# Performance work log

Measured on AMD Instinct MI355X. Metric: run time of the kernel, lower is better.

## Reference

```python
import jax, jax.numpy as jnp
import numpy as np

B, S, D, L = 4, 512, 768, 64


def setup_inputs() -> dict:
    key = jax.random.key(0)
    k1, k2, k3, k4, k5 = jax.random.split(key, 5)
    return {
        "head": jax.random.normal(k1, (B, S, D), dtype=jnp.float32),
        "dep": jax.random.normal(k2, (B, S, D), dtype=jnp.float32),
        "label_U_diag": jax.random.normal(k3, (L, D), dtype=jnp.float32) * 0.02,
        "label_W": jax.random.normal(k4, (L, 2 * D), dtype=jnp.float32) * 0.02,
        "label_b": jax.random.normal(k5, (L,), dtype=jnp.float32) * 0.02,
    }


def reference(head, dep, label_U_diag, label_W, label_b):
    # t1[b,l,i,o] = sum_d head[b,i,d] * U[l,d] * dep[b,o,d]  (diag bilinear)
    t1 = jnp.einsum('bid,ld,bod->blio', head, label_U_diag, dep)
    # Linear term: instead of materializing the O(S^2 * 2D) concat tensor,
    # split W into head/dep halves and broadcast-add two O(S*L) matmuls.
    d = head.shape[-1]
    Wh, Wd = label_W[:, :d], label_W[:, d:]
    t2_h = jnp.einsum('bid,ld->bli', head, Wh)  # [B, L, S] (row / head index)
    t2_d = jnp.einsum('bod,ld->blo', dep, Wd)   # [B, L, S] (col / dep index)
    return t1 + t2_h[:, :, :, None] + t2_d[:, :, None, :] + label_b[None, :, None, None]
```

## Files before the change

kernel.cpp:

```cpp
#include <hip/hip_runtime.h>

typedef __bf16 bf16;
typedef __bf16 bf16x8 __attribute__((ext_vector_type(8)));
typedef float  f32x4  __attribute__((ext_vector_type(4)));

#define S 512
#define DD 768
#define LL 64
#define BB 4

__device__ __forceinline__ void async_copy16(const void* g, void* l) {
    __builtin_amdgcn_global_load_lds(
        (const __attribute__((address_space(1))) unsigned int*)g,
        (__attribute__((address_space(3))) unsigned int*)l,
        16, 0, 0);
}

__device__ __forceinline__ bf16x8 scale_cvt(float4 a, float4 b, float4 ua, float4 ub) {
    bf16x8 p;
    p[0] = (bf16)(a.x * ua.x); p[1] = (bf16)(a.y * ua.y);
    p[2] = (bf16)(a.z * ua.z); p[3] = (bf16)(a.w * ua.w);
    p[4] = (bf16)(b.x * ub.x); p[5] = (bf16)(b.y * ub.y);
    p[6] = (bf16)(b.z * ub.z); p[7] = (bf16)(b.w * ub.w);
    return p;
}

__global__ void cvt_dep_kernel(const float* __restrict__ dep, bf16* __restrict__ out) {
    int idx = (blockIdx.x * 256 + threadIdx.x) * 8;
    float4 a = *(const float4*)(dep + idx);
    float4 c = *(const float4*)(dep + idx + 4);
    bf16x8 p;
    p[0] = (bf16)a.x; p[1] = (bf16)a.y; p[2] = (bf16)a.z; p[3] = (bf16)a.w;
    p[4] = (bf16)c.x; p[5] = (bf16)c.y; p[6] = (bf16)c.z; p[7] = (bf16)c.w;
    *(bf16x8*)(out + idx) = p;
}

__global__ void t2_kernel(const float* __restrict__ head, const float* __restrict__ dep,
                          const float* __restrict__ W, const float* __restrict__ bias,
                          float* __restrict__ t2h, float* __restrict__ t2d) {
    __shared__ float Wl[16][DD];
    __shared__ float red[64][4][16];
    int bid = blockIdx.x;
    int sel = bid >> 7;
    int r   = bid & 127;
    int b   = r >> 5;
    int lg  = (r >> 3) & 3;
    int ic  = r & 7;
    const float* src = sel ? dep : head;
    int t = threadIdx.x;

    for (int l16 = 0; l16 < 16; ++l16) {
        const float* wp = W + (size_t)(lg * 16 + l16) * (2 * DD) + sel * DD;
        Wl[l16][t]       = wp[t];
        Wl[l16][t + 256] = wp[t + 256];
        Wl[l16][t + 512] = wp[t + 512];
    }
    __syncthreads();

    int iq = t >> 2, dq = t & 3;
    int i  = ic * 64 + iq;
    const float* rowp = src + (size_t)(b * S + i) * DD;
    float acc[16];
#pragma unroll
    for (int l16 = 0; l16 < 16; ++l16) acc[l16] = 0.f;
    for (int it = 0; it < 48; ++it) {
        int d = dq * 4 + it * 16;
        float4 x = *(const float4*)(rowp + d);
#pragma unroll
        for (int l16 = 0; l16 < 16; ++l16) {
            float4 wv = *(const float4*)&Wl[l16][d];
            acc[l16] += x.x * wv.x + x.y * wv.y + x.z * wv.z + x.w * wv.w;
        }
    }
#pragma unroll
    for (int l16 = 0; l16 < 16; ++l16) red[iq][dq][l16] = acc[l16];
    __syncthreads();

    int iq2 = t >> 2, l4 = t & 3;
    float* dst = sel ? t2d : t2h;
#pragma unroll
    for (int j = 0; j < 4; ++j) {
        int l16 = l4 * 4 + j;
        float v = red[iq2][0][l16] + red[iq2][1][l16] + red[iq2][2][l16] + red[iq2][3][l16];
        if (sel) v += bias[lg * 16 + l16];
        dst[(size_t)(b * LL + lg * 16 + l16) * S + ic * 64 + iq2] = v;
    }
}

__global__ __launch_bounds__(256, 2) void biaffine_main(
    const float* __restrict__ head, const bf16* __restrict__ depb,
    const float* __restrict__ U, const float* __restrict__ t2h,
    const float* __restrict__ t2d, float* __restrict__ out) {
    __shared__ __align__(16) bf16 As[128][32];
    __shared__ __align__(16) bf16 Bs[128][32];
    __shared__ __align__(16) float Ulds[DD];

    const int tid  = threadIdx.x;
    const int lane = tid & 63;
    const int w    = tid >> 6;
    const int bi0  = (blockIdx.x & 3) << 7;
    const int bo0  = (blockIdx.x >> 2) << 7;
    const int l    = blockIdx.y;
    const int b    = blockIdx.z;

    {
        const float* up = U + (size_t)l * DD;
        Ulds[tid]       = up[tid];
        Ulds[tid + 256] = up[tid + 256];
        Ulds[tid + 512] = up[tid + 512];
    }

    const int r1 = tid >> 2;
    const int cp = tid & 3;
    const int sw = (r1 >> 1) & 3;
    const int ca = cp ^ sw;
    const float* hp0 = head + (size_t)(b * S + bi0 + r1) * DD + ca * 8;
    const float* hp1 = hp0 + (size_t)64 * DD;
    bf16* awr0 = &As[r1][cp * 8];
    bf16* awr1 = &As[r1 + 64][cp * 8];

    const int rB0 = w * 32 + (lane >> 2);
    const int rB1 = rB0 + 16;
    const int cpB = lane & 3;
    const bf16* bp0 = depb + (size_t)(b * S + bo0 + rB0) * DD + (cpB ^ ((rB0 >> 1) & 3)) * 8;
    const bf16* bp1 = depb + (size_t)(b * S + bo0 + rB1) * DD + (cpB ^ ((rB1 >> 1) & 3)) * 8;
    bf16* bw0 = &Bs[w * 32][0];
    bf16* bw1 = &Bs[w * 32 + 16][0];

    const int wr = w & 1, wc = w >> 1;
    const int mrow = lane & 15, q = lane >> 4;
    const bf16* ap[4];
    const bf16* bp[4];
#pragma unroll
    for (int mi = 0; mi < 4; ++mi) {
        int rowA = wr * 64 + mi * 16 + mrow;
        ap[mi] = &As[rowA][(q ^ ((rowA >> 1) & 3)) * 8];
        int rowB = wc * 64 + mi * 16 + mrow;
        bp[mi] = &Bs[rowB][(q ^ ((rowB >> 1) & 3)) * 8];
    }

    f32x4 acc[4][4];
#pragma unroll
    for (int mi = 0; mi < 4; ++mi)
#pragma unroll
        for (int ni = 0; ni < 4; ++ni)
            acc[mi][ni] = (f32x4){0.f, 0.f, 0.f, 0.f};

    __syncthreads();

    const float* h0 = hp0;
    const float* h1 = hp1;
    const bf16*  g0 = bp0;
    const bf16*  g1 = bp1;
    for (int kt = 0; kt < 24; ++kt) {
        float4 h0a = *(const float4*)(h0);
        float4 h0b = *(const float4*)(h0 + 4);
        float4 h1a = *(const float4*)(h1);
        float4 h1b = *(const float4*)(h1 + 4);
        async_copy16(g0, bw0);
        async_copy16(g1, bw1);
        const float* uu = &Ulds[kt * 32 + ca * 8];
        float4 ua = *(const float4*)(uu);
        float4 ub = *(const float4*)(uu + 4);
        *(bf16x8*)awr0 = scale_cvt(h0a, h0b, ua, ub);
        *(bf16x8*)awr1 = scale_cvt(h1a, h1b, ua, ub);
        h0 += 32; h1 += 32; g0 += 32; g1 += 32;
        __syncthreads();

        bf16x8 af[4], bfr[4];
#pragma unroll
        for (int mi = 0; mi < 4; ++mi) af[mi]  = *(const bf16x8*)ap[mi];
#pragma unroll
        for (int ni = 0; ni < 4; ++ni) bfr[ni] = *(const bf16x8*)bp[ni];
#pragma unroll
        for (int mi = 0; mi < 4; ++mi)
#pragma unroll
            for (int ni = 0; ni < 4; ++ni)
                acc[mi][ni] = __builtin_amdgcn_mfma_f32_16x16x32_bf16(af[mi], bfr[ni], acc[mi][ni], 0, 0, 0);
        __syncthreads();
    }

    const size_t bl = (size_t)(b * LL + l);
    const float* t2hp = t2h + bl * S + bi0 + wr * 64;
    const float* t2dp = t2d + bl * S + bo0 + wc * 64;
    float* outbase = out + bl * S * S;
#pragma unroll
    for (int mi = 0; mi < 4; ++mi) {
        float4 th = *(const float4*)&t2hp[mi * 16 + q * 4];
        int row0 = bi0 + wr * 64 + mi * 16 + q * 4;
#pragma unroll
        for (int ni = 0; ni < 4; ++ni) {
            int col = bo0 + wc * 64 + ni * 16 + mrow;
            float td = t2dp[ni * 16 + mrow];
            float* op = outbase + (size_t)row0 * S + col;
            op[0 * S] = acc[mi][ni][0] + th.x + td;
            op[1 * S] = acc[mi][ni][1] + th.y + td;
            op[2 * S] = acc[mi][ni][2] + th.z + td;
            op[3 * S] = acc[mi][ni][3] + th.w + td;
        }
    }
}

extern "C" void kernel_launch(void* const* d_in, const int* in_sizes, int n_in,
                              void* d_out, int out_size, void* d_ws, size_t ws_size,
                              hipStream_t stream) {
    const float* head = (const float*)d_in[0];
    const float* dep  = (const float*)d_in[1];
    const float* U    = (const float*)d_in[2];
    const float* W    = (const float*)d_in[3];
    const float* bias = (const float*)d_in[4];
    float* out = (float*)d_out;

    char*  ws   = (char*)d_ws;
    bf16*  depb = (bf16*)ws;
    float* t2h  = (float*)(ws + 3145728);
    float* t2d  = (float*)(ws + 3145728 + 524288);

    cvt_dep_kernel<<<768, 256, 0, stream>>>(dep, depb);
    t2_kernel<<<256, 256, 0, stream>>>(head, dep, W, bias, t2h, t2d);
    biaffine_main<<<dim3(16, LL, BB), 256, 0, stream>>>(head, depb, U, t2h, t2d, out);
}
```

Before: 398.1 us.

## Enlarge biaffine tile to 256x256 with double-buffered LDS and phased MFMA schedule

```diff
diff --git a/kernel.cpp b/kernel.cpp
--- a/kernel.cpp
+++ b/kernel.cpp
@@ -8,6 +8,7 @@
 #define DD 768
 #define LL 64
 #define BB 4
+#define NKT 12
 
 __device__ __forceinline__ void async_copy16(const void* g, void* l) {
     __builtin_amdgcn_global_load_lds(
@@ -87,107 +88,184 @@
     }
 }
 
-__global__ __launch_bounds__(256, 2) void biaffine_main(
+template<int MH>
+__device__ __forceinline__ void load_a(bf16x8 (&aF)[8], const bf16* Ac, int offA0, int offA1) {
+#pragma unroll
+    for (int mi = 0; mi < 4; ++mi) {
+        aF[mi * 2 + 0] = *(const bf16x8*)(Ac + offA0 + (MH * 4 + mi) * 1024);
+        aF[mi * 2 + 1] = *(const bf16x8*)(Ac + offA1 + (MH * 4 + mi) * 1024);
+    }
+}
+
+template<int NH>
+__device__ __forceinline__ void load_b(bf16x8 (&bFr)[8], const bf16* Bc, int offB0, int offB1) {
+#pragma unroll
+    for (int ni = 0; ni < 2; ++ni) {
+        bFr[(NH * 2 + ni) * 2 + 0] = *(const bf16x8*)(Bc + offB0 + (NH * 2 + ni) * 1024);
+        bFr[(NH * 2 + ni) * 2 + 1] = *(const bf16x8*)(Bc + offB1 + (NH * 2 + ni) * 1024);
+    }
+}
+
+template<int MH, int NH>
+__device__ __forceinline__ void do_mfma(f32x4 (&acc)[8][4], const bf16x8 (&aF)[8], const bf16x8 (&bFr)[8]) {
+#pragma unroll
+    for (int mi = 0; mi < 4; ++mi)
+#pragma unroll
+        for (int ni = 0; ni < 2; ++ni)
+#pragma unroll
+            for (int ks = 0; ks < 2; ++ks)
+                acc[MH * 4 + mi][NH * 2 + ni] = __builtin_amdgcn_mfma_f32_16x16x32_bf16(
+                    aF[mi * 2 + ks], bFr[(NH * 2 + ni) * 2 + ks],
+                    acc[MH * 4 + mi][NH * 2 + ni], 0, 0, 0);
+}
+
+#define PHASE_BEGIN() do { __builtin_amdgcn_s_barrier(); \
+    asm volatile("s_waitcnt lgkmcnt(0)" ::: "memory"); \
+    __builtin_amdgcn_s_setprio(1); } while (0)
+#define PHASE_END() do { __builtin_amdgcn_s_setprio(0); \
+    __builtin_amdgcn_s_barrier(); } while (0)
+
+__global__ __launch_bounds__(512, 2) void biaffine_main(
     const float* __restrict__ head, const bf16* __restrict__ depb,
     const float* __restrict__ U, const float* __restrict__ t2h,
     const float* __restrict__ t2d, float* __restrict__ out) {
-    __shared__ __align__(16) bf16 As[128][32];
-    __shared__ __align__(16) bf16 Bs[128][32];
+    __shared__ __align__(16) bf16 As[2][256][64];
+    __shared__ __align__(16) bf16 Bs[2][256][64];
     __shared__ __align__(16) float Ulds[DD];
 
     const int tid  = threadIdx.x;
     const int lane = tid & 63;
     const int w    = tid >> 6;
-    const int bi0  = (blockIdx.x & 3) << 7;
-    const int bo0  = (blockIdx.x >> 2) << 7;
+    const int bi0  = (blockIdx.x & 1) << 8;
+    const int bo0  = (blockIdx.x >> 1) << 8;
     const int l    = blockIdx.y;
     const int b    = blockIdx.z;
 
-    {
-        const float* up = U + (size_t)l * DD;
-        Ulds[tid]       = up[tid];
-        Ulds[tid + 256] = up[tid + 256];
-        Ulds[tid + 512] = up[tid + 512];
-    }
-
-    const int r1 = tid >> 2;
-    const int cp = tid & 3;
-    const int sw = (r1 >> 1) & 3;
-    const int ca = cp ^ sw;
-    const float* hp0 = head + (size_t)(b * S + bi0 + r1) * DD + ca * 8;
-    const float* hp1 = hp0 + (size_t)64 * DD;
-    bf16* awr0 = &As[r1][cp * 8];
-    bf16* awr1 = &As[r1 + 64][cp * 8];
-
-    const int rB0 = w * 32 + (lane >> 2);
-    const int rB1 = rB0 + 16;
-    const int cpB = lane & 3;
-    const bf16* bp0 = depb + (size_t)(b * S + bo0 + rB0) * DD + (cpB ^ ((rB0 >> 1) & 3)) * 8;
-    const bf16* bp1 = depb + (size_t)(b * S + bo0 + rB1) * DD + (cpB ^ ((rB1 >> 1) & 3)) * 8;
-    bf16* bw0 = &Bs[w * 32][0];
-    bf16* bw1 = &Bs[w * 32 + 16][0];
+    bf16* AsB = &As[0][0][0];
+    bf16* BsB = &Bs[0][0][0];
+
+    Ulds[tid] = U[(size_t)l * DD + tid];
+    if (tid < DD - 512) Ulds[512 + tid] = U[(size_t)l * DD + 512 + tid];
+
+    const int arow = tid >> 1;
+    const int ach  = tid & 1;
+    const float* hp = head + (size_t)(b * S + bi0 + arow) * DD + ach * 32;
+    const int as7 = arow & 7;
+    const int wr0 = arow * 64 + (((ach * 4 + 0) ^ as7) * 8);
+    const int wr1 = arow * 64 + (((ach * 4 + 1) ^ as7) * 8);
+    const int wr2 = arow * 64 + (((ach * 4 + 2) ^ as7) * 8);
+    const int wr3 = arow * 64 + (((ach * 4 + 3) ^ as7) * 8);
+
+    const int brg = lane >> 3;
+    const int bsl = lane & 7;
+    const bf16* bsrc0 = depb + (size_t)(b * S + bo0 +   0 + w * 8 + brg) * DD + ((bsl ^ brg) * 8);
+    const bf16* bsrc1 = depb + (size_t)(b * S + bo0 +  64 + w * 8 + brg) * DD + ((bsl ^ brg) * 8);
+    const bf16* bsrc2 = depb + (size_t)(b * S + bo0 + 128 + w * 8 + brg) * DD + ((bsl ^ brg) * 8);
+    const bf16* bsrc3 = depb + (size_t)(b * S + bo0 + 192 + w * 8 + brg) * DD + ((bsl ^ brg) * 8);
+    bf16* BwB0 = &Bs[0][  0 + w * 8][0];
+    bf16* BwB1 = &Bs[0][ 64 + w * 8][0];
+    bf16* BwB2 = &Bs[0][128 + w * 8][0];
+    bf16* BwB3 = &Bs[0][192 + w * 8][0];
 
     const int wr = w & 1, wc = w >> 1;
     const int mrow = lane & 15, q = lane >> 4;
-    const bf16* ap[4];
-    const bf16* bp[4];
-#pragma unroll
-    for (int mi = 0; mi < 4; ++mi) {
-        int rowA = wr * 64 + mi * 16 + mrow;
-        ap[mi] = &As[rowA][(q ^ ((rowA >> 1) & 3)) * 8];
-        int rowB = wc * 64 + mi * 16 + mrow;
-        bp[mi] = &Bs[rowB][(q ^ ((rowB >> 1) & 3)) * 8];
-    }
-
-    f32x4 acc[4][4];
-#pragma unroll
-    for (int mi = 0; mi < 4; ++mi)
+    const int sw = mrow & 7;
+    const int offA0 = (wr * 128 + mrow) * 64 + ((q ^ sw) * 8);
+    const int offA1 = (wr * 128 + mrow) * 64 + (((4 + q) ^ sw) * 8);
+    const int offB0 = (wc * 64 + mrow) * 64 + ((q ^ sw) * 8);
+    const int offB1 = (wc * 64 + mrow) * 64 + (((4 + q) ^ sw) * 8);
+
+    f32x4 acc[8][4];
+#pragma unroll
+    for (int mi = 0; mi < 8; ++mi)
 #pragma unroll
         for (int ni = 0; ni < 4; ++ni)
             acc[mi][ni] = (f32x4){0.f, 0.f, 0.f, 0.f};
 
+    bf16x8 aF[8], bFr[8];
+    float4 aLd0, aLd1, aLd2, aLd3, aLd4, aLd5, aLd6, aLd7;
+
+    aLd0 = *(const float4*)(hp +  0); aLd1 = *(const float4*)(hp +  4);
+    aLd2 = *(const float4*)(hp +  8); aLd3 = *(const float4*)(hp + 12);
+    aLd4 = *(const float4*)(hp + 16); aLd5 = *(const float4*)(hp + 20);
+    aLd6 = *(const float4*)(hp + 24); aLd7 = *(const float4*)(hp + 28);
+    async_copy16(bsrc0, BwB0);
+    async_copy16(bsrc1, BwB1);
+    async_copy16(bsrc2, BwB2);
+    async_copy16(bsrc3, BwB3);
     __syncthreads();
-
-    const float* h0 = hp0;
-    const float* h1 = hp1;
-    const bf16*  g0 = bp0;
-    const bf16*  g1 = bp1;
-    for (int kt = 0; kt < 24; ++kt) {
-        float4 h0a = *(const float4*)(h0);
-        float4 h0b = *(const float4*)(h0 + 4);
-        float4 h1a = *(const float4*)(h1);
-        float4 h1b = *(const float4*)(h1 + 4);
-        async_copy16(g0, bw0);
-        async_copy16(g1, bw1);
-        const float* uu = &Ulds[kt * 32 + ca * 8];
-        float4 ua = *(const float4*)(uu);
-        float4 ub = *(const float4*)(uu + 4);
-        *(bf16x8*)awr0 = scale_cvt(h0a, h0b, ua, ub);
-        *(bf16x8*)awr1 = scale_cvt(h1a, h1b, ua, ub);
-        h0 += 32; h1 += 32; g0 += 32; g1 += 32;
-        __syncthreads();
-
-        bf16x8 af[4], bfr[4];
-#pragma unroll
-        for (int mi = 0; mi < 4; ++mi) af[mi]  = *(const bf16x8*)ap[mi];
-#pragma unroll
-        for (int ni = 0; ni < 4; ++ni) bfr[ni] = *(const bf16x8*)bp[ni];
-#pragma unroll
-        for (int mi = 0; mi < 4; ++mi)
-#pragma unroll
-            for (int ni = 0; ni < 4; ++ni)
-                acc[mi][ni] = __builtin_amdgcn_mfma_f32_16x16x32_bf16(af[mi], bfr[ni], acc[mi][ni], 0, 0, 0);
-        __syncthreads();
+    {
+        const float* up = &Ulds[ach * 32];
+        bf16* Aw = AsB;
+        float4 u0, u1; bf16x8 pk;
+        u0 = *(const float4*)(up +  0); u1 = *(const float4*)(up +  4);
+        pk = scale_cvt(aLd0, aLd1, u0, u1); *(bf16x8*)(Aw + wr0) = pk;
+        u0 = *(const float4*)(up +  8); u1 = *(const float4*)(up + 12);
+        pk = scale_cvt(aLd2, aLd3, u0, u1); *(bf16x8*)(Aw + wr1) = pk;
+        u0 = *(const float4*)(up + 16); u1 = *(const float4*)(up + 20);
+        pk = scale_cvt(aLd4, aLd5, u0, u1); *(bf16x8*)(Aw + wr2) = pk;
+        u0 = *(const float4*)(up + 24); u1 = *(const float4*)(up + 28);
+        pk = scale_cvt(aLd6, aLd7, u0, u1); *(bf16x8*)(Aw + wr3) = pk;
+    }
+    __syncthreads();
+
+#pragma unroll 2
+    for (int kt = 0; kt < NKT; ++kt) {
+        const int c = kt & 1;
+        const int s = c ^ 1;
+        const bool st = (kt < NKT - 1);
+        const int kt1 = kt + 1;
+        const bf16* Ac = AsB + c * 16384;
+        const bf16* Bc = BsB + c * 16384;
+        bf16* Aw = AsB + s * 16384;
+        const float* hpt = hp + kt1 * 64;
+
+        load_a<0>(aF, Ac, offA0, offA1);
+        load_b<0>(bFr, Bc, offB0, offB1);
+        if (st) {
+            aLd0 = *(const float4*)(hpt +  0); aLd1 = *(const float4*)(hpt +  4);
+            aLd2 = *(const float4*)(hpt +  8); aLd3 = *(const float4*)(hpt + 12);
+            async_copy16(bsrc0 + kt1 * 64, BwB0 + s * 16384);
+            async_copy16(bsrc1 + kt1 * 64, BwB1 + s * 16384);
+        }
+        PHASE_BEGIN(); do_mfma<0, 0>(acc, aF, bFr); PHASE_END();
+
+        load_b<1>(bFr, Bc, offB0, offB1);
+        if (st) {
+            aLd4 = *(const float4*)(hpt + 16); aLd5 = *(const float4*)(hpt + 20);
+            aLd6 = *(const float4*)(hpt + 24); aLd7 = *(const float4*)(hpt + 28);
+            async_copy16(bsrc2 + kt1 * 64, BwB2 + s * 16384);
+            async_copy16(bsrc3 + kt1 * 64, BwB3 + s * 16384);
+        }
+        PHASE_BEGIN(); do_mfma<0, 1>(acc, aF, bFr); PHASE_END();
+
+        load_a<1>(aF, Ac, offA0, offA1);
+        if (st) {
+            const float* up = &Ulds[kt1 * 64 + ach * 32];
+            float4 u0, u1; bf16x8 pk;
+            u0 = *(const float4*)(up +  0); u1 = *(const float4*)(up +  4);
+            pk = scale_cvt(aLd0, aLd1, u0, u1); *(bf16x8*)(Aw + wr0) = pk;
+            u0 = *(const float4*)(up +  8); u1 = *(const float4*)(up + 12);
+            pk = scale_cvt(aLd2, aLd3, u0, u1); *(bf16x8*)(Aw + wr1) = pk;
+            u0 = *(const float4*)(up + 16); u1 = *(const float4*)(up + 20);
+            pk = scale_cvt(aLd4, aLd5, u0, u1); *(bf16x8*)(Aw + wr2) = pk;
+            u0 = *(const float4*)(up + 24); u1 = *(const float4*)(up + 28);
+            pk = scale_cvt(aLd6, aLd7, u0, u1); *(bf16x8*)(Aw + wr3) = pk;
+        }
+        PHASE_BEGIN(); do_mfma<1, 1>(acc, aF, bFr); PHASE_END();
+
+        if (st) asm volatile("s_waitcnt vmcnt(0)" ::: "memory");
+        PHASE_BEGIN(); do_mfma<1, 0>(acc, aF, bFr); PHASE_END();
     }
 
     const size_t bl = (size_t)(b * LL + l);
-    const float* t2hp = t2h + bl * S + bi0 + wr * 64;
+    const float* t2hp = t2h + bl * S + bi0 + wr * 128;
     const float* t2dp = t2d + bl * S + bo0 + wc * 64;
-    float* outbase = out + bl * S * S;
-#pragma unroll
-    for (int mi = 0; mi < 4; ++mi) {
+    float* outbase = out + bl * (size_t)(S * S);
+#pragma unroll
+    for (int mi = 0; mi < 8; ++mi) {
         float4 th = *(const float4*)&t2hp[mi * 16 + q * 4];
-        int row0 = bi0 + wr * 64 + mi * 16 + q * 4;
+        int row0 = bi0 + wr * 128 + mi * 16 + q * 4;
 #pragma unroll
         for (int ni = 0; ni < 4; ++ni) {
             int col = bo0 + wc * 64 + ni * 16 + mrow;
@@ -218,5 +296,5 @@
 
     cvt_dep_kernel<<<768, 256, 0, stream>>>(dep, depb);
     t2_kernel<<<256, 256, 0, stream>>>(head, dep, W, bias, t2h, t2d);
-    biaffine_main<<<dim3(16, LL, BB), 256, 0, stream>>>(head, depb, U, t2h, t2d, out);
-}
+    biaffine_main<<<dim3(4, LL, BB), 512, 0, stream>>>(head, depb, U, t2h, t2d, out);
+}
```

Measured after the change: 501.2 us. 1.26x slower.

## Double-buffer LDS tiles in biaffine main loop to overlap loads with MFMA

Applied to the files above, without the earlier changes.

```diff
diff --git a/kernel.cpp b/kernel.cpp
--- a/kernel.cpp
+++ b/kernel.cpp
@@ -87,12 +87,12 @@
     }
 }
 
-__global__ __launch_bounds__(256, 2) void biaffine_main(
+__global__ __launch_bounds__(256, 3) void biaffine_main(
     const float* __restrict__ head, const bf16* __restrict__ depb,
     const float* __restrict__ U, const float* __restrict__ t2h,
     const float* __restrict__ t2d, float* __restrict__ out) {
-    __shared__ __align__(16) bf16 As[128][32];
-    __shared__ __align__(16) bf16 Bs[128][32];
+    __shared__ __align__(16) bf16 As[2][128][32];
+    __shared__ __align__(16) bf16 Bs[2][128][32];
     __shared__ __align__(16) float Ulds[DD];
 
     const int tid  = threadIdx.x;
@@ -103,6 +103,9 @@
     const int l    = blockIdx.y;
     const int b    = blockIdx.z;
 
+    bf16* AsB = &As[0][0][0];
+    bf16* BsB = &Bs[0][0][0];
+
     {
         const float* up = U + (size_t)l * DD;
         Ulds[tid]       = up[tid];
@@ -116,27 +119,26 @@
     const int ca = cp ^ sw;
     const float* hp0 = head + (size_t)(b * S + bi0 + r1) * DD + ca * 8;
     const float* hp1 = hp0 + (size_t)64 * DD;
-    bf16* awr0 = &As[r1][cp * 8];
-    bf16* awr1 = &As[r1 + 64][cp * 8];
+    const int aoff0 = r1 * 32 + cp * 8;
+    const int aoff1 = (r1 + 64) * 32 + cp * 8;
 
     const int rB0 = w * 32 + (lane >> 2);
     const int rB1 = rB0 + 16;
     const int cpB = lane & 3;
-    const bf16* bp0 = depb + (size_t)(b * S + bo0 + rB0) * DD + (cpB ^ ((rB0 >> 1) & 3)) * 8;
-    const bf16* bp1 = depb + (size_t)(b * S + bo0 + rB1) * DD + (cpB ^ ((rB1 >> 1) & 3)) * 8;
-    bf16* bw0 = &Bs[w * 32][0];
-    bf16* bw1 = &Bs[w * 32 + 16][0];
+    const bf16* bg0 = depb + (size_t)(b * S + bo0 + rB0) * DD + (cpB ^ ((rB0 >> 1) & 3)) * 8;
+    const bf16* bg1 = depb + (size_t)(b * S + bo0 + rB1) * DD + (cpB ^ ((rB1 >> 1) & 3)) * 8;
+    const int boff0 = (w * 32) * 32;
+    const int boff1 = (w * 32 + 16) * 32;
 
     const int wr = w & 1, wc = w >> 1;
     const int mrow = lane & 15, q = lane >> 4;
-    const bf16* ap[4];
-    const bf16* bp[4];
+    int aFo[4], bFo[4];
 #pragma unroll
     for (int mi = 0; mi < 4; ++mi) {
         int rowA = wr * 64 + mi * 16 + mrow;
-        ap[mi] = &As[rowA][(q ^ ((rowA >> 1) & 3)) * 8];
+        aFo[mi] = rowA * 32 + ((q ^ ((rowA >> 1) & 3)) * 8);
         int rowB = wc * 64 + mi * 16 + mrow;
-        bp[mi] = &Bs[rowB][(q ^ ((rowB >> 1) & 3)) * 8];
+        bFo[mi] = rowB * 32 + ((q ^ ((rowB >> 1) & 3)) * 8);
     }
 
     f32x4 acc[4][4];
@@ -146,44 +148,63 @@
         for (int ni = 0; ni < 4; ++ni)
             acc[mi][ni] = (f32x4){0.f, 0.f, 0.f, 0.f};
 
-    __syncthreads();
-
-    const float* h0 = hp0;
-    const float* h1 = hp1;
-    const bf16*  g0 = bp0;
-    const bf16*  g1 = bp1;
-    for (int kt = 0; kt < 24; ++kt) {
-        float4 h0a = *(const float4*)(h0);
-        float4 h0b = *(const float4*)(h0 + 4);
-        float4 h1a = *(const float4*)(h1);
-        float4 h1b = *(const float4*)(h1 + 4);
-        async_copy16(g0, bw0);
-        async_copy16(g1, bw1);
-        const float* uu = &Ulds[kt * 32 + ca * 8];
+    float4 h0a = *(const float4*)(hp0);
+    float4 h0b = *(const float4*)(hp0 + 4);
+    float4 h1a = *(const float4*)(hp1);
+    float4 h1b = *(const float4*)(hp1 + 4);
+    async_copy16(bg0, BsB + boff0);
+    async_copy16(bg1, BsB + boff1);
+    __syncthreads();
+    {
+        const float* uu = &Ulds[ca * 8];
         float4 ua = *(const float4*)(uu);
         float4 ub = *(const float4*)(uu + 4);
-        *(bf16x8*)awr0 = scale_cvt(h0a, h0b, ua, ub);
-        *(bf16x8*)awr1 = scale_cvt(h1a, h1b, ua, ub);
-        h0 += 32; h1 += 32; g0 += 32; g1 += 32;
-        __syncthreads();
+        *(bf16x8*)(AsB + aoff0) = scale_cvt(h0a, h0b, ua, ub);
+        *(bf16x8*)(AsB + aoff1) = scale_cvt(h1a, h1b, ua, ub);
+    }
+    __syncthreads();
+
+    for (int kt = 0; kt < 24; ++kt) {
+        const int coff = (kt & 1) * 4096;
+        const int soff = coff ^ 4096;
+        const bool st = kt < 23;
+
+        if (st) {
+            const float* h0 = hp0 + (kt + 1) * 32;
+            const float* h1 = hp1 + (kt + 1) * 32;
+            h0a = *(const float4*)(h0);
+            h0b = *(const float4*)(h0 + 4);
+            h1a = *(const float4*)(h1);
+            h1b = *(const float4*)(h1 + 4);
+            async_copy16(bg0 + (kt + 1) * 32, BsB + soff + boff0);
+            async_copy16(bg1 + (kt + 1) * 32, BsB + soff + boff1);
+        }
 
         bf16x8 af[4], bfr[4];
 #pragma unroll
-        for (int mi = 0; mi < 4; ++mi) af[mi]  = *(const bf16x8*)ap[mi];
-#pragma unroll
-        for (int ni = 0; ni < 4; ++ni) bfr[ni] = *(const bf16x8*)bp[ni];
+        for (int mi = 0; mi < 4; ++mi) af[mi]  = *(const bf16x8*)(AsB + coff + aFo[mi]);
+#pragma unroll
+        for (int ni = 0; ni < 4; ++ni) bfr[ni] = *(const bf16x8*)(BsB + coff + bFo[ni]);
 #pragma unroll
         for (int mi = 0; mi < 4; ++mi)
 #pragma unroll
             for (int ni = 0; ni < 4; ++ni)
                 acc[mi][ni] = __builtin_amdgcn_mfma_f32_16x16x32_bf16(af[mi], bfr[ni], acc[mi][ni], 0, 0, 0);
+
+        if (st) {
+            const float* uu = &Ulds[(kt + 1) * 32 + ca * 8];
+            float4 ua = *(const float4*)(uu);
+            float4 ub = *(const float4*)(uu + 4);
+            *(bf16x8*)(AsB + soff + aoff0) = scale_cvt(h0a, h0b, ua, ub);
+            *(bf16x8*)(AsB + soff + aoff1) = scale_cvt(h1a, h1b, ua, ub);
+        }
         __syncthreads();
     }
 
     const size_t bl = (size_t)(b * LL + l);
     const float* t2hp = t2h + bl * S + bi0 + wr * 64;
     const float* t2dp = t2d + bl * S + bo0 + wc * 64;
-    float* outbase = out + bl * S * S;
+    float* outbase = out + bl * (size_t)(S * S);
 #pragma unroll
     for (int mi = 0; mi < 4; ++mi) {
         float4 th = *(const float4*)&t2hp[mi * 16 + q * 4];
```

Result: faster. 389.4 us (-2.2%).
